# Kernel tuning notes

Measured on AMD Instinct MI355X. Metric: run time of the kernel, lower is better.

Reference implementation:

```python
import jax, jax.numpy as jnp
import numpy as np

NUM_HEADS = 16
THETA = 10000.0


def _rope(x):
    # x: [b, h, s, d_k], interleaved-pair RoPE
    s, d = x.shape[-2], x.shape[-1]
    inv_freq = 1.0 / (THETA ** (jnp.arange(0, d, 2, dtype=jnp.float32) / d))  # [d/2]
    ang = jnp.arange(s, dtype=jnp.float32)[:, None] * inv_freq[None, :]       # [s, d/2]
    cos = jnp.repeat(jnp.cos(ang), 2, axis=-1)[None, None]                    # [1,1,s,d]
    sin = jnp.repeat(jnp.sin(ang), 2, axis=-1)[None, None]
    x_even = x[..., 0::2]
    x_odd = x[..., 1::2]
    rot = jnp.stack((-x_odd, x_even), axis=-1).reshape(x.shape)
    return x * cos.astype(x.dtype) + rot * sin.astype(x.dtype)


def setup_inputs() -> dict:
    key = jax.random.key(0)
    ks = jax.random.split(key, 5)
    b, s, d = 4, 2048, 1024
    std = (2.0 / (d + d)) ** 0.5
    return {
        "x": jax.random.normal(ks[0], (b, s, d), dtype=jnp.float32),
        "wq": jax.random.normal(ks[1], (d, d), dtype=jnp.float32) * std,
        "wk": jax.random.normal(ks[2], (d, d), dtype=jnp.float32) * std,
        "wv": jax.random.normal(ks[3], (d, d), dtype=jnp.float32) * std,
        "wo": jax.random.normal(ks[4], (d, d), dtype=jnp.float32) * std,
    }


def reference(x, wq, wk, wv, wo):
    b, s, d_model = x.shape
    h = NUM_HEADS
    d_k = d_model // h

    def proj(w):
        y = jnp.einsum('bsd,od->bso', x, w)
        return y.reshape(b, s, h, d_k).transpose(0, 2, 1, 3)  # [b,h,s,d_k]

    q = _rope(proj(wq))
    k = _rope(proj(wk))
    v = proj(wv)

    scores = jnp.einsum('bhqd,bhkd->bhqk', q, k) / (d_k ** 0.5)
    causal = jnp.tril(jnp.ones((s, s), dtype=bool))[None, None]
    scores = jnp.where(causal, scores, -jnp.inf)
    attn = jax.nn.softmax(scores, axis=-1)
    out = jnp.einsum('bhqk,bhkd->bhqd', attn, v)
    out = out.transpose(0, 2, 1, 3).reshape(b, s, d_model)
    return jnp.einsum('bsd,od->bso', out, wo)
```

## Files before the change

kernel.cpp:

```cpp
#include <hip/hip_runtime.h>
#include <stdint.h>

#define NHEAD  16
#define SEQ    2048
#define DMODEL 1024
#define BATCH  4

typedef __attribute__((ext_vector_type(4))) float f32x4;
typedef __attribute__((ext_vector_type(8))) __bf16 bf16x8;
typedef __attribute__((ext_vector_type(8))) unsigned short u16x8;

__device__ __forceinline__ unsigned short f2bf(float f) {
    unsigned int u = __builtin_bit_cast(unsigned int, f);
    u += 0x7FFFu + ((u >> 16) & 1u);
    return (unsigned short)(u >> 16);
}

__device__ __forceinline__ unsigned int cvt_pk_bf16(float lo, float hi) {
    unsigned int r;
    asm("v_cvt_pk_bf16_f32 %0, %1, %2" : "=v"(r) : "v"(lo), "v"(hi));
    return r;
}

__device__ __forceinline__ float max3f(float a, float b, float c) {
    float d;
    asm("v_max3_f32 %0, %1, %2, %3" : "=v"(d) : "v"(a), "v"(b), "v"(c));
    return d;
}

__device__ __forceinline__ void gload_lds16(const void* g, void* l) {
    __builtin_amdgcn_global_load_lds(
        (const __attribute__((address_space(1))) unsigned int*)(uintptr_t)g,
        (__attribute__((address_space(3))) unsigned int*)(uintptr_t)l,
        16, 0, 0);
}

__device__ __forceinline__ bf16x8 lds_frag(const unsigned short* p) {
    return __builtin_bit_cast(bf16x8, *(const u16x8*)p);
}

__device__ __forceinline__ bf16x8 gfrag(const unsigned short* p) {
    return __builtin_bit_cast(bf16x8, *(const u16x8*)p);
}

__global__ __launch_bounds__(256) void cvt_all(const float* __restrict__ x,
                                               const float* __restrict__ w0,
                                               const float* __restrict__ w1,
                                               const float* __restrict__ w2,
                                               const float* __restrict__ w3,
                                               unsigned short* __restrict__ xb,
                                               unsigned short* __restrict__ wdst) {
    int b = blockIdx.x;
    const float* src;
    unsigned short* dst;
    int i;
    if (b < 8192) {
        src = x; dst = xb;
        i = b * 256 + threadIdx.x;
    } else {
        int wb = b - 8192;
        int which = wb >> 10;
        src = which == 0 ? w0 : which == 1 ? w1 : which == 2 ? w2 : w3;
        dst = wdst + (size_t)which * 1024 * 1024;
        i = (wb & 1023) * 256 + threadIdx.x;
    }
    float4 v = ((const float4*)src)[i];
    ushort4 o;
    o.x = f2bf(v.x); o.y = f2bf(v.y); o.z = f2bf(v.z); o.w = f2bf(v.w);
    ((ushort4*)dst)[i] = o;
}

__global__ __launch_bounds__(256) void gemm_qkv(const unsigned short* __restrict__ A,
                                                const unsigned short* __restrict__ Wc,
                                                unsigned short* __restrict__ qw,
                                                unsigned short* __restrict__ kw,
                                                unsigned short* __restrict__ vw) {
    __shared__ __align__(16) unsigned short As[2][128 * 64];
    __shared__ __align__(16) unsigned short Bs[2][128 * 64];

    const int tid  = threadIdx.x;
    const int lane = tid & 63;
    const int wid  = tid >> 6;
    const int wm = wid >> 1, wn = wid & 1;
    const int l15 = lane & 15, lg = lane >> 4;

    const int tn = blockIdx.x;
    const int m0 = blockIdx.y * 128, n0 = tn * 128;

    f32x4 acc[4][4];
#pragma unroll
    for (int i = 0; i < 4; i++)
#pragma unroll
        for (int j = 0; j < 4; j++) acc[i][j] = f32x4{0.f, 0.f, 0.f, 0.f};

    const int e0 = tid * 8;
    auto STAGE = [&](int kk, int bufi) {
#pragma unroll
        for (int is = 0; is < 4; ++is) {
            int e = is * 2048 + e0;
            int row = e >> 6, col = e & 63;
            gload_lds16(A  + (size_t)(m0 + row) * 1024 + kk + col, &As[bufi][e]);
            gload_lds16(Wc + (size_t)(n0 + row) * 1024 + kk + col, &Bs[bufi][e]);
        }
    };

    STAGE(0, 0);
    __syncthreads();

    for (int kk = 0; kk < 1024; kk += 64) {
        const int cur = (kk >> 6) & 1;
        if (kk + 64 < 1024) STAGE(kk + 64, cur ^ 1);
#pragma unroll
        for (int ks = 0; ks < 2; ++ks) {
            bf16x8 a[4], b[4];
#pragma unroll
            for (int f = 0; f < 4; f++) {
                a[f] = lds_frag(&As[cur][(wm * 64 + f * 16 + l15) * 64 + ks * 32 + lg * 8]);
                b[f] = lds_frag(&Bs[cur][(wn * 64 + f * 16 + l15) * 64 + ks * 32 + lg * 8]);
            }
#pragma unroll
            for (int i = 0; i < 4; i++)
#pragma unroll
                for (int j = 0; j < 4; j++)
                    acc[i][j] = __builtin_amdgcn_mfma_f32_16x16x32_bf16(a[i], b[j], acc[i][j], 0, 0, 0);
        }
        __syncthreads();
    }

    if (tn >= 16) {
        unsigned short* out = vw;
#pragma unroll
        for (int i = 0; i < 4; i++)
#pragma unroll
            for (int r = 0; r < 4; r++) {
                int m = m0 + wm * 64 + i * 16 + lg * 4 + r;
                int b = m >> 11, s = m & 2047;
#pragma unroll
                for (int j = 0; j < 4; j++) {
                    int n = n0 + wn * 64 + j * 16 + l15;
                    int h = (n >> 6) & 15, dk = n & 63;
                    out[((size_t)(b * NHEAD + h) * 64 + dk) * SEQ + s] = f2bf(acc[i][j][r]);
                }
            }
    } else {
        unsigned short* out = (tn < 8) ? qw : kw;
        const float qscale = (tn < 8) ? 0.18033688011112042f : 1.0f;
        const float L2T = 13.287712379549449f;
        float invf[4];
#pragma unroll
        for (int j = 0; j < 4; j++) {
            int idx = j * 16 + l15;
            int t = idx >> 1;
            invf[j] = exp2f(-((float)(2 * t) * (1.0f / 64.0f)) * L2T);
        }
        const int par = l15 & 1;
#pragma unroll
        for (int i = 0; i < 4; i++)
#pragma unroll
            for (int r = 0; r < 4; r++) {
                int m = m0 + wm * 64 + i * 16 + lg * 4 + r;
                int b = m >> 11, s = m & 2047;
                float fs = (float)s;
#pragma unroll
                for (int j = 0; j < 4; j++) {
                    float v = acc[i][j][r];
                    float other = __shfl_xor(v, 1);
                    float sn, cs;
                    __sincosf(fs * invf[j], &sn, &cs);
                    float y = par ? fmaf(v, cs, other * sn) : fmaf(v, cs, -other * sn);
                    y *= qscale;
                    int n = n0 + wn * 64 + j * 16 + l15;
                    int h = (n >> 6) & 15, dk = n & 63;
                    out[((size_t)(b * NHEAD + h) * SEQ + s) * 64 + dk] = f2bf(y);
                }
            }
    }
}

__global__ __launch_bounds__(256) void gemm_out(const unsigned short* __restrict__ A,
                                                const unsigned short* __restrict__ W,
                                                float* __restrict__ out) {
    __shared__ __align__(16) unsigned short As[2][128 * 64];
    __shared__ __align__(16) unsigned short Bs[2][128 * 64];

    const int tid  = threadIdx.x;
    const int lane = tid & 63;
    const int wid  = tid >> 6;
    const int wm = wid >> 1, wn = wid & 1;
    const int l15 = lane & 15, lg = lane >> 4;

    const int tn = blockIdx.x & 7;
    const int tm = blockIdx.x >> 3;
    const int m0 = tm * 128, n0 = tn * 128;

    f32x4 acc[4][4];
#pragma unroll
    for (int i = 0; i < 4; i++)
#pragma unroll
        for (int j = 0; j < 4; j++) acc[i][j] = f32x4{0.f, 0.f, 0.f, 0.f};

    const int e0 = tid * 8;
    auto STAGE = [&](int kk, int bufi) {
#pragma unroll
        for (int is = 0; is < 4; ++is) {
            int e = is * 2048 + e0;
            int row = e >> 6, col = e & 63;
            gload_lds16(A + (size_t)(m0 + row) * 1024 + kk + col, &As[bufi][e]);
            gload_lds16(W + (size_t)(n0 + row) * 1024 + kk + col, &Bs[bufi][e]);
        }
    };

    STAGE(0, 0);
    __syncthreads();

    for (int kk = 0; kk < 1024; kk += 64) {
        const int cur = (kk >> 6) & 1;
        if (kk + 64 < 1024) STAGE(kk + 64, cur ^ 1);
#pragma unroll
        for (int ks = 0; ks < 2; ++ks) {
            bf16x8 a[4], b[4];
#pragma unroll
            for (int f = 0; f < 4; f++) {
                a[f] = lds_frag(&As[cur][(wm * 64 + f * 16 + l15) * 64 + ks * 32 + lg * 8]);
                b[f] = lds_frag(&Bs[cur][(wn * 64 + f * 16 + l15) * 64 + ks * 32 + lg * 8]);
            }
#pragma unroll
            for (int i = 0; i < 4; i++)
#pragma unroll
                for (int j = 0; j < 4; j++)
                    acc[i][j] = __builtin_amdgcn_mfma_f32_16x16x32_bf16(a[i], b[j], acc[i][j], 0, 0, 0);
        }
        __syncthreads();
    }

#pragma unroll
    for (int i = 0; i < 4; i++)
#pragma unroll
        for (int r = 0; r < 4; r++) {
            int m = m0 + wm * 64 + i * 16 + lg * 4 + r;
            float* orow = out + (size_t)m * 1024 + n0 + wn * 64 + l15;
#pragma unroll
            for (int j = 0; j < 4; j++) orow[j * 16] = acc[i][j][r];
        }
}

__global__ __launch_bounds__(256, 4) void flash_attn(const unsigned short* __restrict__ Qw,
                                                     const unsigned short* __restrict__ Kw,
                                                     const unsigned short* __restrict__ Vw,
                                                     unsigned short* __restrict__ Ow) {
    __shared__ __align__(16) unsigned short Ks[2][64 * 64];
    __shared__ __align__(16) unsigned short Vs[2][64 * 64];
    __shared__ __align__(16) unsigned short Ps[64 * 64];

    const int tid  = threadIdx.x;
    const int lane = tid & 63;
    const int w    = tid >> 6;
    const int l15 = lane & 15, lg = lane >> 4;
    const int l7 = l15 & 7;

    const int logical = (blockIdx.x & 7) * 128 + (blockIdx.x >> 3);
    const int bh = logical >> 4;
    const int p  = logical & 15;
    const int qbB = 31 - p;

    const unsigned short* Kbh = Kw + (size_t)bh * (SEQ * 64);
    const unsigned short* Vbh = Vw + (size_t)bh * (64 * SEQ);

    const int qrow0 = w * 16;
    const int prow  = qrow0 + l15;

    const unsigned short* QrowA = Qw + (size_t)bh * (SEQ * 64) + (size_t)(p * 64 + prow) * 64;
    const unsigned short* QrowB = Qw + (size_t)bh * (SEQ * 64) + (size_t)(qbB * 64 + prow) * 64;
    bf16x8 qA0 = gfrag(QrowA + lg * 8), qA1 = gfrag(QrowA + 32 + lg * 8);
    bf16x8 qB0 = gfrag(QrowB + lg * 8), qB1 = gfrag(QrowB + 32 + lg * 8);

    u16x8 onesu = {0x3F80, 0x3F80, 0x3F80, 0x3F80, 0x3F80, 0x3F80, 0x3F80, 0x3F80};
    const bf16x8 vones = __builtin_bit_cast(bf16x8, onesu);

    auto STAGE = [&](int kt2, int bufi) {
#pragma unroll
        for (int is = 0; is < 2; ++is) {
            int e = (is * 256 + tid) * 8;
            int row = e >> 6, c = (e >> 3) & 7;
            int sc = (c ^ (row & 7)) << 3;
            gload_lds16(Kbh + (size_t)kt2 * 4096 + row * 64 + sc, &Ks[bufi][e]);
            gload_lds16(Vbh + (size_t)row * SEQ + kt2 * 64 + sc, &Vs[bufi][e]);
        }
    };

    STAGE(0, 0);

    f32x4 oaccA[4], oaccB[4];
#pragma unroll
    for (int f = 0; f < 4; f++) { oaccA[f] = f32x4{0.f, 0.f, 0.f, 0.f}; oaccB[f] = f32x4{0.f, 0.f, 0.f, 0.f}; }
    f32x4 accA5 = f32x4{0.f, 0.f, 0.f, 0.f}, accB5 = f32x4{0.f, 0.f, 0.f, 0.f};
    float mA = 0.f, mB = 0.f;

    unsigned short* pbase = &Ps[prow * 64];
    const unsigned short* prd = &Ps[prow * 64];

    int cur = 0;
    __syncthreads();

    auto PROC = [&](bf16x8 q0, bf16x8 q1, f32x4* oacc, f32x4& acc5, float& mrun, bool diag) {
        f32x4 st[4];
        const f32x4 cinit = {-mrun, -mrun, -mrun, -mrun};
        __builtin_amdgcn_s_setprio(1);
#pragma unroll
        for (int f = 0; f < 4; f++) {
            bf16x8 kfrag = lds_frag(&Ks[cur][(f * 16 + l15) * 64 + ((lg ^ l7) << 3)]);
            st[f] = __builtin_amdgcn_mfma_f32_16x16x32_bf16(kfrag, q0, cinit, 0, 0, 0);
        }
#pragma unroll
        for (int f = 0; f < 4; f++) {
            bf16x8 kfrag = lds_frag(&Ks[cur][(f * 16 + l15) * 64 + (((4 + lg) ^ l7) << 3)]);
            st[f] = __builtin_amdgcn_mfma_f32_16x16x32_bf16(kfrag, q1, st[f], 0, 0, 0);
        }
        __builtin_amdgcn_s_setprio(0);

        if (diag) {
#pragma unroll
            for (int f = 0; f < 4; f++)
#pragma unroll
                for (int r = 0; r < 4; r++) {
                    int kv = f * 16 + 4 * lg + r;
                    if (kv > prow) st[f][r] = -3.0e38f;
                }
        }

        float m1 = max3f(st[0][0], st[0][1], st[0][2]);
        float m2 = max3f(st[0][3], st[1][0], st[1][1]);
        float m3 = max3f(st[1][2], st[1][3], st[2][0]);
        float m4 = max3f(st[2][1], st[2][2], st[2][3]);
        float m5 = max3f(st[3][0], st[3][1], st[3][2]);
        float pm = fmaxf(max3f(m1, m2, m3), max3f(m4, m5, st[3][3]));
        pm = fmaxf(pm, __shfl_xor(pm, 16));
        pm = fmaxf(pm, __shfl_xor(pm, 32));

        if (!__all(pm <= 8.0f)) {
            float d = fmaxf(pm, 0.0f);
            float sc0 = exp2f(-d);
            mrun += d;
#pragma unroll
            for (int f = 0; f < 4; f++)
#pragma unroll
                for (int r = 0; r < 4; r++) st[f][r] -= d;
#pragma unroll
            for (int r = 0; r < 4; r++) {
                float so = __shfl(sc0, lg * 4 + r);
#pragma unroll
                for (int f = 0; f < 4; f++) oacc[f][r] *= so;
                acc5[r] *= so;
            }
        }

#pragma unroll
        for (int f = 0; f < 4; f++)
#pragma unroll
            for (int r = 0; r < 4; r++)
                st[f][r] = exp2f(st[f][r]);

        {
            const int halfoff = (lg & 1) << 2;
            const int cbase = lg >> 1;
#pragma unroll
            for (int f = 0; f < 4; f++) {
                uint2 pw;
                pw.x = cvt_pk_bf16(st[f][0], st[f][1]);
                pw.y = cvt_pk_bf16(st[f][2], st[f][3]);
                *(uint2*)(pbase + (((2 * f + cbase) ^ l7) << 3) + halfoff) = pw;
            }
        }

        __builtin_amdgcn_s_setprio(1);
#pragma unroll
        for (int ks = 0; ks < 2; ++ks) {
            bf16x8 pa = lds_frag(prd + (((ks * 4 + lg) ^ l7) << 3));
#pragma unroll
            for (int f = 0; f < 4; f++) {
                bf16x8 vb = lds_frag(&Vs[cur][(f * 16 + l15) * 64 + (((ks * 4 + lg) ^ l7) << 3)]);
                oacc[f] = __builtin_amdgcn_mfma_f32_16x16x32_bf16(pa, vb, oacc[f], 0, 0, 0);
            }
            acc5 = __builtin_amdgcn_mfma_f32_16x16x32_bf16(pa, vones, acc5, 0, 0, 0);
        }
        __builtin_amdgcn_s_setprio(0);
    };

    for (int kt = 0; kt <= p; ++kt) {
        if (kt < p) STAGE(kt + 1, cur ^ 1);
        else        STAGE(0, cur ^ 1);
        PROC(qA0, qA1, oaccA, accA5, mA, kt == p);
        __syncthreads();
        cur ^= 1;
    }
    for (int kt = 0; kt <= qbB; ++kt) {
        if (kt < qbB) STAGE(kt + 1, cur ^ 1);
        PROC(qB0, qB1, oaccB, accB5, mB, kt == qbB);
        __syncthreads();
        cur ^= 1;
    }

    const int b = bh >> 4, h = bh & 15;
#pragma unroll
    for (int r = 0; r < 4; r++) {
        float invA = 1.0f / accA5[r];
        int sgA = p * 64 + qrow0 + lg * 4 + r;
        unsigned short* orowA = Ow + ((size_t)(b * SEQ + sgA) * DMODEL) + h * 64 + l15;
#pragma unroll
        for (int f = 0; f < 4; f++) orowA[f * 16] = f2bf(oaccA[f][r] * invA);

        float invB = 1.0f / accB5[r];
        int sgB = qbB * 64 + qrow0 + lg * 4 + r;
        unsigned short* orowB = Ow + ((size_t)(b * SEQ + sgB) * DMODEL) + h * 64 + l15;
#pragma unroll
        for (int f = 0; f < 4; f++) orowB[f * 16] = f2bf(oaccB[f][r] * invB);
    }
}

extern "C" void kernel_launch(void* const* d_in, const int* in_sizes, int n_in,
                              void* d_out, int out_size, void* d_ws, size_t ws_size,
                              hipStream_t stream) {
    const float* x  = (const float*)d_in[0];
    const float* wq = (const float*)d_in[1];
    const float* wk = (const float*)d_in[2];
    const float* wv = (const float*)d_in[3];
    const float* wo = (const float*)d_in[4];

    unsigned short* ws = (unsigned short*)d_ws;
    const size_t MEL = (size_t)8192 * 1024;
    const size_t WEL = (size_t)1024 * 1024;
    unsigned short* xb  = ws;
    unsigned short* wqb = xb + MEL;
    unsigned short* wob = wqb + 3 * WEL;
    unsigned short* qw  = wob + WEL;
    unsigned short* kw  = qw + MEL;
    unsigned short* vw  = kw + MEL;
    unsigned short* ow  = vw + MEL;

    cvt_all<<<12288, 256, 0, stream>>>(x, wq, wk, wv, wo, xb, wqb);

    gemm_qkv<<<dim3(24, 64), 256, 0, stream>>>(xb, wqb, qw, kw, vw);

    flash_attn<<<1024, 256, 0, stream>>>(qw, kw, vw, ow);

    gemm_out<<<512, 256, 0, stream>>>(ow, wob, (float*)d_out);
}
```

Measured before the change: 177.7 us.

## Rewrite QKV GEMM as 256x256-tile, 8-wave, swizzled-LDS ping-pong pipeline

Replaces the 128x128, 4-wave QKV projection GEMM with a 256x256-tile, 512-thread kernel using 128KB of dynamic LDS. Staging is split into half-tiles, and each wave runs a multi-phase schedule that interleaves global-to-LDS loads with MFMA bursts, using explicit barriers, waitcnts and setprio. A XOR swizzle on LDS columns is meant to avoid bank conflicts. The aim is more data reuse per tile and better overlap of memory with compute. The cost is one block per CU, a grid of only 384 blocks, and a fragile hand-written schedule.

```diff
diff --git a/kernel.cpp b/kernel.cpp
--- a/kernel.cpp
+++ b/kernel.cpp
@@ -70,95 +70,279 @@
     ((ushort4*)dst)[i] = o;
 }
 
-__global__ __launch_bounds__(256) void gemm_qkv(const unsigned short* __restrict__ A,
-                                                const unsigned short* __restrict__ Wc,
-                                                unsigned short* __restrict__ qw,
-                                                unsigned short* __restrict__ kw,
-                                                unsigned short* __restrict__ vw) {
-    __shared__ __align__(16) unsigned short As[2][128 * 64];
-    __shared__ __align__(16) unsigned short Bs[2][128 * 64];
+__global__ __launch_bounds__(512, 1) void gemm8_qkv(const unsigned short* __restrict__ A,
+                                                    const unsigned short* __restrict__ Wc,
+                                                    unsigned short* __restrict__ qw,
+                                                    unsigned short* __restrict__ kw,
+                                                    unsigned short* __restrict__ vw) {
+    extern __shared__ __align__(16) unsigned short lds[];
 
     const int tid  = threadIdx.x;
     const int lane = tid & 63;
     const int wid  = tid >> 6;
-    const int wm = wid >> 1, wn = wid & 1;
-    const int l15 = lane & 15, lg = lane >> 4;
-
-    const int tn = blockIdx.x;
-    const int m0 = blockIdx.y * 128, n0 = tn * 128;
-
-    f32x4 acc[4][4];
-#pragma unroll
-    for (int i = 0; i < 4; i++)
+    const int wm = wid >> 2, wn = wid & 3;
+    const int l15 = lane & 15, lg = lane >> 4, l7 = l15 & 7;
+
+    const int bx = blockIdx.x;
+    const int m0 = blockIdx.y * 256;
+    const int n0 = bx * 256;
+
+    auto STAGE_A = [&](int t, int h) {
+        unsigned short* dst = lds + ((t & 1) * 2 + h) * 8192;
+#pragma unroll
+        for (int pass = 0; pass < 2; ++pass) {
+            int ci = pass * 512 + tid;
+            int row = ci >> 3, c = ci & 7;
+            gload_lds16(A + (size_t)(m0 + h * 128 + row) * 1024 + t * 64 + ((c ^ (row & 7)) << 3),
+                        dst + ci * 8);
+        }
+    };
+    auto STAGE_B = [&](int t, int h) {
+        unsigned short* dst = lds + 32768 + ((t & 1) * 2 + h) * 8192;
+#pragma unroll
+        for (int pass = 0; pass < 2; ++pass) {
+            int ci = pass * 512 + tid;
+            int row = ci >> 3, c = ci & 7;
+            gload_lds16(Wc + (size_t)(n0 + h * 128 + row) * 1024 + t * 64 + ((c ^ (row & 7)) << 3),
+                        dst + ci * 8);
+        }
+    };
+
+    f32x4 acc[8][4];
+#pragma unroll
+    for (int i = 0; i < 8; i++)
 #pragma unroll
         for (int j = 0; j < 4; j++) acc[i][j] = f32x4{0.f, 0.f, 0.f, 0.f};
 
-    const int e0 = tid * 8;
-    auto STAGE = [&](int kk, int bufi) {
-#pragma unroll
-        for (int is = 0; is < 4; ++is) {
-            int e = is * 2048 + e0;
-            int row = e >> 6, col = e & 63;
-            gload_lds16(A  + (size_t)(m0 + row) * 1024 + kk + col, &As[bufi][e]);
-            gload_lds16(Wc + (size_t)(n0 + row) * 1024 + kk + col, &Bs[bufi][e]);
-        }
-    };
-
-    STAGE(0, 0);
-    __syncthreads();
-
-    for (int kk = 0; kk < 1024; kk += 64) {
-        const int cur = (kk >> 6) & 1;
-        if (kk + 64 < 1024) STAGE(kk + 64, cur ^ 1);
-#pragma unroll
-        for (int ks = 0; ks < 2; ++ks) {
-            bf16x8 a[4], b[4];
-#pragma unroll
-            for (int f = 0; f < 4; f++) {
-                a[f] = lds_frag(&As[cur][(wm * 64 + f * 16 + l15) * 64 + ks * 32 + lg * 8]);
-                b[f] = lds_frag(&Bs[cur][(wn * 64 + f * 16 + l15) * 64 + ks * 32 + lg * 8]);
-            }
-#pragma unroll
-            for (int i = 0; i < 4; i++)
-#pragma unroll
-                for (int j = 0; j < 4; j++)
-                    acc[i][j] = __builtin_amdgcn_mfma_f32_16x16x32_bf16(a[i], b[j], acc[i][j], 0, 0, 0);
-        }
-        __syncthreads();
+    const int aoff = (wm * 64 + l15) * 64;
+    const int boff = (wn * 32 + l15) * 64;
+    const int cs0 = (lg ^ l7) << 3;
+    const int cs1 = ((4 + lg) ^ l7) << 3;
+
+    bf16x8 a8[8], b0[4], b1[4];
+
+    STAGE_A(0, 0); STAGE_B(0, 0); STAGE_B(0, 1); STAGE_A(0, 1);
+    STAGE_A(1, 0); STAGE_B(1, 0); STAGE_B(1, 1);
+    asm volatile("s_waitcnt vmcnt(6)" ::: "memory");
+    __builtin_amdgcn_sched_barrier(0);
+    __builtin_amdgcn_s_barrier();
+
+    for (int it = 0; it < 8; ++it) {
+        const int T0 = 2 * it, T1 = 2 * it + 1;
+        const bool notlast = (it != 7);
+
+        {
+            const unsigned short* As_ = lds;
+            const unsigned short* Bs_ = lds + 32768;
+#pragma unroll
+            for (int q = 0; q < 4; q++) {
+                a8[q * 2 + 0] = lds_frag(As_ + aoff + q * 1024 + cs0);
+                a8[q * 2 + 1] = lds_frag(As_ + aoff + q * 1024 + cs1);
+            }
+#pragma unroll
+            for (int s = 0; s < 2; s++) {
+                b0[s * 2 + 0] = lds_frag(Bs_ + boff + s * 1024 + cs0);
+                b0[s * 2 + 1] = lds_frag(Bs_ + boff + s * 1024 + cs1);
+            }
+            STAGE_A(T1, 1);
+            __builtin_amdgcn_s_barrier();
+            asm volatile("s_waitcnt lgkmcnt(0)" ::: "memory");
+            __builtin_amdgcn_sched_barrier(0);
+            __builtin_amdgcn_s_setprio(1);
+#pragma unroll
+            for (int q = 0; q < 4; q++)
+#pragma unroll
+                for (int s = 0; s < 2; s++) {
+                    acc[q][s] = __builtin_amdgcn_mfma_f32_16x16x32_bf16(a8[q*2+0], b0[s*2+0], acc[q][s], 0, 0, 0);
+                    acc[q][s] = __builtin_amdgcn_mfma_f32_16x16x32_bf16(a8[q*2+1], b0[s*2+1], acc[q][s], 0, 0, 0);
+                }
+            __builtin_amdgcn_s_setprio(0);
+            __builtin_amdgcn_s_barrier();
+        }
+        {
+            const unsigned short* Bs_ = lds + 32768 + 8192;
+#pragma unroll
+            for (int s = 0; s < 2; s++) {
+                b1[s * 2 + 0] = lds_frag(Bs_ + boff + s * 1024 + cs0);
+                b1[s * 2 + 1] = lds_frag(Bs_ + boff + s * 1024 + cs1);
+            }
+            if (notlast) STAGE_A(T0 + 2, 0);
+            __builtin_amdgcn_s_barrier();
+            asm volatile("s_waitcnt lgkmcnt(0)" ::: "memory");
+            __builtin_amdgcn_sched_barrier(0);
+            __builtin_amdgcn_s_setprio(1);
+#pragma unroll
+            for (int q = 0; q < 4; q++)
+#pragma unroll
+                for (int s = 0; s < 2; s++) {
+                    acc[q][2+s] = __builtin_amdgcn_mfma_f32_16x16x32_bf16(a8[q*2+0], b1[s*2+0], acc[q][2+s], 0, 0, 0);
+                    acc[q][2+s] = __builtin_amdgcn_mfma_f32_16x16x32_bf16(a8[q*2+1], b1[s*2+1], acc[q][2+s], 0, 0, 0);
+                }
+            __builtin_amdgcn_s_setprio(0);
+            __builtin_amdgcn_s_barrier();
+        }
+        {
+            const unsigned short* As_ = lds + 8192;
+#pragma unroll
+            for (int q = 0; q < 4; q++) {
+                a8[q * 2 + 0] = lds_frag(As_ + aoff + q * 1024 + cs0);
+                a8[q * 2 + 1] = lds_frag(As_ + aoff + q * 1024 + cs1);
+            }
+            if (notlast) STAGE_B(T0 + 2, 0);
+            __builtin_amdgcn_s_barrier();
+            asm volatile("s_waitcnt lgkmcnt(0)" ::: "memory");
+            __builtin_amdgcn_sched_barrier(0);
+            __builtin_amdgcn_s_setprio(1);
+#pragma unroll
+            for (int q = 0; q < 4; q++)
+#pragma unroll
+                for (int s = 0; s < 2; s++) {
+                    acc[4+q][2+s] = __builtin_amdgcn_mfma_f32_16x16x32_bf16(a8[q*2+0], b1[s*2+0], acc[4+q][2+s], 0, 0, 0);
+                    acc[4+q][2+s] = __builtin_amdgcn_mfma_f32_16x16x32_bf16(a8[q*2+1], b1[s*2+1], acc[4+q][2+s], 0, 0, 0);
+                }
+            __builtin_amdgcn_s_setprio(0);
+            __builtin_amdgcn_s_barrier();
+        }
+        {
+            if (notlast) STAGE_B(T0 + 2, 1);
+            __builtin_amdgcn_s_barrier();
+            __builtin_amdgcn_s_setprio(1);
+#pragma unroll
+            for (int q = 0; q < 4; q++)
+#pragma unroll
+                for (int s = 0; s < 2; s++) {
+                    acc[4+q][s] = __builtin_amdgcn_mfma_f32_16x16x32_bf16(a8[q*2+0], b0[s*2+0], acc[4+q][s], 0, 0, 0);
+                    acc[4+q][s] = __builtin_amdgcn_mfma_f32_16x16x32_bf16(a8[q*2+1], b0[s*2+1], acc[4+q][s], 0, 0, 0);
+                }
+            __builtin_amdgcn_s_setprio(0);
+            if (notlast) { asm volatile("s_waitcnt vmcnt(6)" ::: "memory"); }
+            else         { asm volatile("s_waitcnt vmcnt(0)" ::: "memory"); }
+            __builtin_amdgcn_sched_barrier(0);
+            __builtin_amdgcn_s_barrier();
+        }
+        {
+            const unsigned short* As_ = lds + 2 * 8192;
+            const unsigned short* Bs_ = lds + 32768 + 2 * 8192;
+#pragma unroll
+            for (int q = 0; q < 4; q++) {
+                a8[q * 2 + 0] = lds_frag(As_ + aoff + q * 1024 + cs0);
+                a8[q * 2 + 1] = lds_frag(As_ + aoff + q * 1024 + cs1);
+            }
+#pragma unroll
+            for (int s = 0; s < 2; s++) {
+                b0[s * 2 + 0] = lds_frag(Bs_ + boff + s * 1024 + cs0);
+                b0[s * 2 + 1] = lds_frag(Bs_ + boff + s * 1024 + cs1);
+            }
+            if (notlast) STAGE_A(T0 + 2, 1);
+            __builtin_amdgcn_s_barrier();
+            asm volatile("s_waitcnt lgkmcnt(0)" ::: "memory");
+            __builtin_amdgcn_sched_barrier(0);
+            __builtin_amdgcn_s_setprio(1);
+#pragma unroll
+            for (int q = 0; q < 4; q++)
+#pragma unroll
+                for (int s = 0; s < 2; s++) {
+                    acc[q][s] = __builtin_amdgcn_mfma_f32_16x16x32_bf16(a8[q*2+0], b0[s*2+0], acc[q][s], 0, 0, 0);
+                    acc[q][s] = __builtin_amdgcn_mfma_f32_16x16x32_bf16(a8[q*2+1], b0[s*2+1], acc[q][s], 0, 0, 0);
+                }
+            __builtin_amdgcn_s_setprio(0);
+            __builtin_amdgcn_s_barrier();
+        }
+        {
+            const unsigned short* Bs_ = lds + 32768 + 3 * 8192;
+#pragma unroll
+            for (int s = 0; s < 2; s++) {
+                b1[s * 2 + 0] = lds_frag(Bs_ + boff + s * 1024 + cs0);
+                b1[s * 2 + 1] = lds_frag(Bs_ + boff + s * 1024 + cs1);
+            }
+            if (notlast) STAGE_A(T1 + 2, 0);
+            __builtin_amdgcn_s_barrier();
+            asm volatile("s_waitcnt lgkmcnt(0)" ::: "memory");
+            __builtin_amdgcn_sched_barrier(0);
+            __builtin_amdgcn_s_setprio(1);
+#pragma unroll
+            for (int q = 0; q < 4; q++)
+#pragma unroll
+                for (int s = 0; s < 2; s++) {
+                    acc[q][2+s] = __builtin_amdgcn_mfma_f32_16x16x32_bf16(a8[q*2+0], b1[s*2+0], acc[q][2+s], 0, 0, 0);
+                    acc[q][2+s] = __builtin_amdgcn_mfma_f32_16x16x32_bf16(a8[q*2+1], b1[s*2+1], acc[q][2+s], 0, 0, 0);
+                }
+            __builtin_amdgcn_s_setprio(0);
+            __builtin_amdgcn_s_barrier();
+        }
+        {
+            const unsigned short* As_ = lds + 3 * 8192;
+#pragma unroll
+            for (int q = 0; q < 4; q++) {
+                a8[q * 2 + 0] = lds_frag(As_ + aoff + q * 1024 + cs0);
+                a8[q * 2 + 1] = lds_frag(As_ + aoff + q * 1024 + cs1);
+            }
+            if (notlast) STAGE_B(T1 + 2, 0);
+            __builtin_amdgcn_s_barrier();
+            asm volatile("s_waitcnt lgkmcnt(0)" ::: "memory");
+            __builtin_amdgcn_sched_barrier(0);
+            __builtin_amdgcn_s_setprio(1);
+#pragma unroll
+            for (int q = 0; q < 4; q++)
+#pragma unroll
+                for (int s = 0; s < 2; s++) {
+                    acc[4+q][2+s] = __builtin_amdgcn_mfma_f32_16x16x32_bf16(a8[q*2+0], b1[s*2+0], acc[4+q][2+s], 0, 0, 0);
+                    acc[4+q][2+s] = __builtin_amdgcn_mfma_f32_16x16x32_bf16(a8[q*2+1], b1[s*2+1], acc[4+q][2+s], 0, 0, 0);
+                }
+            __builtin_amdgcn_s_setprio(0);
+            __builtin_amdgcn_s_barrier();
+        }
+        {
+            if (notlast) STAGE_B(T1 + 2, 1);
+            __builtin_amdgcn_s_barrier();
+            __builtin_amdgcn_s_setprio(1);
+#pragma unroll
+            for (int q = 0; q < 4; q++)
+#pragma unroll
+                for (int s = 0; s < 2; s++) {
+                    acc[4+q][s] = __builtin_amdgcn_mfma_f32_16x16x32_bf16(a8[q*2+0], b0[s*2+0], acc[4+q][s], 0, 0, 0);
+                    acc[4+q][s] = __builtin_amdgcn_mfma_f32_16x16x32_bf16(a8[q*2+1], b0[s*2+1], acc[4+q][s], 0, 0, 0);
+                }
+            __builtin_amdgcn_s_setprio(0);
+            if (notlast) { asm volatile("s_waitcnt vmcnt(6)" ::: "memory"); }
+            else         { asm volatile("s_waitcnt vmcnt(0)" ::: "memory"); }
+            __builtin_amdgcn_sched_barrier(0);
+            __builtin_amdgcn_s_barrier();
+        }
     }
 
-    if (tn >= 16) {
-        unsigned short* out = vw;
-#pragma unroll
-        for (int i = 0; i < 4; i++)
+    const int opnd = bx >> 2;
+    if (opnd == 2) {
+#pragma unroll
+        for (int i = 0; i < 8; i++)
 #pragma unroll
             for (int r = 0; r < 4; r++) {
-                int m = m0 + wm * 64 + i * 16 + lg * 4 + r;
+                int m = m0 + (i >> 2) * 128 + wm * 64 + (i & 3) * 16 + lg * 4 + r;
                 int b = m >> 11, s = m & 2047;
 #pragma unroll
                 for (int j = 0; j < 4; j++) {
-                    int n = n0 + wn * 64 + j * 16 + l15;
-                    int h = (n >> 6) & 15, dk = n & 63;
-                    out[((size_t)(b * NHEAD + h) * 64 + dk) * SEQ + s] = f2bf(acc[i][j][r]);
+                    int n_op = (bx & 3) * 256 + (j >> 1) * 128 + wn * 32 + (j & 1) * 16 + l15;
+                    int h = n_op >> 6, dk = n_op & 63;
+                    vw[((size_t)(b * NHEAD + h) * 64 + dk) * SEQ + s] = f2bf(acc[i][j][r]);
                 }
             }
     } else {
-        unsigned short* out = (tn < 8) ? qw : kw;
-        const float qscale = (tn < 8) ? 0.18033688011112042f : 1.0f;
+        unsigned short* out = (opnd == 0) ? qw : kw;
+        const float qscale = (opnd == 0) ? 0.18033688011112042f : 1.0f;
         const float L2T = 13.287712379549449f;
         float invf[4];
 #pragma unroll
         for (int j = 0; j < 4; j++) {
-            int idx = j * 16 + l15;
+            int idx = (wn & 1) * 32 + (j & 1) * 16 + l15;
             int t = idx >> 1;
             invf[j] = exp2f(-((float)(2 * t) * (1.0f / 64.0f)) * L2T);
         }
         const int par = l15 & 1;
 #pragma unroll
-        for (int i = 0; i < 4; i++)
+        for (int i = 0; i < 8; i++)
 #pragma unroll
             for (int r = 0; r < 4; r++) {
-                int m = m0 + wm * 64 + i * 16 + lg * 4 + r;
+                int m = m0 + (i >> 2) * 128 + wm * 64 + (i & 3) * 16 + lg * 4 + r;
                 int b = m >> 11, s = m & 2047;
                 float fs = (float)s;
 #pragma unroll
@@ -169,8 +353,8 @@
                     __sincosf(fs * invf[j], &sn, &cs);
                     float y = par ? fmaf(v, cs, other * sn) : fmaf(v, cs, -other * sn);
                     y *= qscale;
-                    int n = n0 + wn * 64 + j * 16 + l15;
-                    int h = (n >> 6) & 15, dk = n & 63;
+                    int n_op = (bx & 3) * 256 + (j >> 1) * 128 + wn * 32 + (j & 1) * 16 + l15;
+                    int h = n_op >> 6, dk = n_op & 63;
                     out[((size_t)(b * NHEAD + h) * SEQ + s) * 64 + dk] = f2bf(y);
                 }
             }
@@ -437,9 +621,13 @@
     unsigned short* vw  = kw + MEL;
     unsigned short* ow  = vw + MEL;
 
+    const int QKV_LDS = 131072;
+    (void)hipFuncSetAttribute((const void*)gemm8_qkv,
+                              hipFuncAttributeMaxDynamicSharedMemorySize, QKV_LDS);
+
     cvt_all<<<12288, 256, 0, stream>>>(x, wq, wk, wv, wo, xb, wqb);
 
-    gemm_qkv<<<dim3(24, 64), 256, 0, stream>>>(xb, wqb, qw, kw, vw);
+    gemm8_qkv<<<dim3(12, 32), 512, QKV_LDS, stream>>>(xb, wqb, qw, kw, vw);
 
     flash_attn<<<1024, 256, 0, stream>>>(qw, kw, vw, ow);
 
```

After: 179.0 us. About the same (+0.7%).
